# Kernel tuning notes

Hardware: AMD Instinct MI355X
Metric: run time of the kernel (lower is better)

The kernel has to match this reference:

```python
import jax, jax.numpy as jnp
import numpy as np

LAMB = 5.0
B, N = 1024, 3125  # batch, anchors (5 anchors x 25x25 map)

def setup_inputs() -> dict:
    key = jax.random.key(0)
    k1, k2, k3, k4 = jax.random.split(key, 4)
    return {
        "c_pred": jax.random.normal(k1, (B, N, 2), dtype=jnp.float32),
        "r_pred": jax.random.normal(k2, (B, N, 4), dtype=jnp.float32),
        "r_target": jax.random.normal(k3, (B, N, 4), dtype=jnp.float32),
        # anchor labels in {-1: ignore, 0: negative, 1: positive}
        "label": jax.random.randint(k4, (B, N), -1, 2, dtype=jnp.int32),
    }

def reference(c_pred, r_pred, r_target, label):
    dt = c_pred.dtype
    pos = (label == 1)
    neg = (label == 0)
    pos_cnt = pos.sum(axis=-1).astype(dt)  # [B]
    neg_cnt = neg.sum(axis=-1).astype(dt)

    # --- classification: masked 2-class cross-entropy, pos/neg balanced per batch ---
    logp = jax.nn.log_softmax(c_pred, axis=-1)  # [B, N, 2]
    ce_pos = -logp[..., 1]                      # CE when target class = 1
    ce_neg = -logp[..., 0]                      # CE when target class = 0
    pos_mean = jnp.where(pos_cnt > 0,
                         (ce_pos * pos).sum(axis=-1) / jnp.maximum(pos_cnt, 1.0), 0.0)
    neg_mean = (ce_neg * neg).sum(axis=-1) / jnp.maximum(neg_cnt, 1.0)
    c_loss = ((pos_mean + neg_mean) * 0.5).mean()

    d = r_pred - r_target
    a = jnp.abs(d)
    sl = jnp.where(a < 1.0, 0.5 * d * d, a - 0.5)  # [B, N, 4]
    # per-batch mean over pos_num*4 elements == masked mean of per-anchor coord-mean
    r_per = (sl.mean(axis=-1) * pos).sum(axis=-1) / jnp.maximum(pos_cnt, 1.0)
    r_loss = jnp.where(pos_cnt > 0, r_per, 0.0).mean()

    t_loss = c_loss + LAMB * r_loss
    return (c_loss, r_loss, t_loss)
```

## Files before the change

### kernel.cpp

```cpp
#include <hip/hip_runtime.h>

#define BATCH 1024
#define NANCH 3125
#define LAMB  5.0f
#define NBLK  (BATCH * 4)

__device__ __forceinline__ float wave_red_f(float v) {
    #pragma unroll
    for (int o = 32; o > 0; o >>= 1) v += __shfl_down(v, o, 64);
    return v;
}

__device__ __forceinline__ float lse2(float cx, float cy) {
    const float m = fmaxf(cx, cy);
    return m + __logf(1.f + __expf(-fabsf(cx - cy)));
}

__device__ __forceinline__ float sl1(float4 p, float4 t) {
    float s4 = 0.f, d, a;
    d = p.x - t.x; a = fabsf(d); s4 += (a < 1.f) ? 0.5f * d * d : a - 0.5f;
    d = p.y - t.y; a = fabsf(d); s4 += (a < 1.f) ? 0.5f * d * d : a - 0.5f;
    d = p.z - t.z; a = fabsf(d); s4 += (a < 1.f) ? 0.5f * d * d : a - 0.5f;
    d = p.w - t.w; a = fabsf(d); s4 += (a < 1.f) ? 0.5f * d * d : a - 0.5f;
    return s4 * 0.25f;
}

__global__ __launch_bounds__(256) void partial_kernel(
    const float* __restrict__ c_pred,
    const float* __restrict__ r_pred,
    const float* __restrict__ r_target,
    const int*   __restrict__ label,
    float*       __restrict__ partial)
{
    const int blk = blockIdx.x;
    const int b   = blk >> 2;
    const int s   = blk & 3;
    const int tid = threadIdx.x;
    const int u   = (s << 8) | tid;

    const int align0  = (4 - (b & 3)) & 3;
    const int ngroups = (NANCH - align0) >> 2;
    const int ntail   = NANCH - align0 - (ngroups << 2);

    const float*  crow = c_pred + (size_t)b * (NANCH * 2);
    const float4* rp   = (const float4*)(r_pred   + (size_t)b * NANCH * 4);
    const float4* rt   = (const float4*)(r_target + (size_t)b * NANCH * 4);
    const int*    lb   = label + (size_t)b * NANCH;

    float cp = 0.f, cn = 0.f, sl = 0.f, pc = 0.f, nc = 0.f;

    if (u < ngroups) {
        const int a = align0 + (u << 2);

        const int4   L   = *(const int4*)(lb + a);
        const float4 C01 = *(const float4*)(crow + 2 * a);
        const float4 C23 = *(const float4*)(crow + 2 * a + 4);

        const bool p0 = (L.x == 1), p1 = (L.y == 1), p2 = (L.z == 1), p3 = (L.w == 1);
        float4 P0, T0, P1, T1, P2, T2, P3, T3;
        if (p0) { P0 = rp[a];     T0 = rt[a];     }
        if (p1) { P1 = rp[a + 1]; T1 = rt[a + 1]; }
        if (p2) { P2 = rp[a + 2]; T2 = rt[a + 2]; }
        if (p3) { P3 = rp[a + 3]; T3 = rt[a + 3]; }

        const float e0 = lse2(C01.x, C01.y), e1 = lse2(C01.z, C01.w);
        const float e2 = lse2(C23.x, C23.y), e3 = lse2(C23.z, C23.w);
        const bool n0 = (L.x == 0), n1 = (L.y == 0), n2 = (L.z == 0), n3 = (L.w == 0);

        pc = (p0 ? 1.f : 0.f) + (p1 ? 1.f : 0.f) + (p2 ? 1.f : 0.f) + (p3 ? 1.f : 0.f);
        nc = (n0 ? 1.f : 0.f) + (n1 ? 1.f : 0.f) + (n2 ? 1.f : 0.f) + (n3 ? 1.f : 0.f);
        cp = (p0 ? (e0 - C01.y) : 0.f) + (p1 ? (e1 - C01.w) : 0.f)
           + (p2 ? (e2 - C23.y) : 0.f) + (p3 ? (e3 - C23.w) : 0.f);
        cn = (n0 ? (e0 - C01.x) : 0.f) + (n1 ? (e1 - C01.z) : 0.f)
           + (n2 ? (e2 - C23.x) : 0.f) + (n3 ? (e3 - C23.z) : 0.f);

        if (p0) sl += sl1(P0, T0);
        if (p1) sl += sl1(P1, T1);
        if (p2) sl += sl1(P2, T2);
        if (p3) sl += sl1(P3, T3);
    } else {
        const int k = u - ngroups;
        const int nextra = align0 + ntail;
        if (k < nextra) {
            const int a = (k < align0) ? k
                        : (align0 + (ngroups << 2) + (k - align0));
            const int   l  = lb[a];
            const float cx = crow[2 * a], cy = crow[2 * a + 1];
            const float e  = lse2(cx, cy);
            if (l == 1) {
                pc = 1.f; cp = e - cy;
                sl = sl1(rp[a], rt[a]);
            } else if (l == 0) {
                nc = 1.f; cn = e - cx;
            }
        }
    }

    cp = wave_red_f(cp);
    cn = wave_red_f(cn);
    sl = wave_red_f(sl);
    pc = wave_red_f(pc);
    nc = wave_red_f(nc);

    __shared__ float sm[5][4];
    const int wid = tid >> 6, lane = tid & 63;
    if (lane == 0) {
        sm[0][wid] = cp; sm[1][wid] = cn; sm[2][wid] = sl;
        sm[3][wid] = pc; sm[4][wid] = nc;
    }
    __syncthreads();
    if (tid < 5) {
        const int k = tid;
        partial[(size_t)blk * 5 + k] = sm[k][0] + sm[k][1] + sm[k][2] + sm[k][3];
    }
}

__global__ __launch_bounds__(512) void finalize_kernel(
    const float* __restrict__ partial,
    float*       __restrict__ out)
{
    const int tid = threadIdx.x;
    float csum = 0.f, rsum = 0.f;

    for (int b = tid; b < BATCH; b += 512) {
        float cp = 0.f, cn = 0.f, sl = 0.f, pc = 0.f, nc = 0.f;
        #pragma unroll
        for (int s = 0; s < 4; ++s) {
            const float* p = partial + ((size_t)b * 4 + s) * 5;
            cp += p[0]; cn += p[1]; sl += p[2]; pc += p[3]; nc += p[4];
        }
        const bool haspos = (pc > 0.5f);
        const float pos_mean = haspos ? cp / pc : 0.f;
        const float neg_mean = cn / fmaxf(nc, 1.f);
        csum += (pos_mean + neg_mean) * 0.5f;
        rsum += haspos ? sl / pc : 0.f;
    }

    csum = wave_red_f(csum);
    rsum = wave_red_f(rsum);

    __shared__ float s_c[8], s_r[8];
    const int wid = tid >> 6, lane = tid & 63;
    if (lane == 0) { s_c[wid] = csum; s_r[wid] = rsum; }
    __syncthreads();
    if (tid == 0) {
        float cs = 0.f, rs = 0.f;
        #pragma unroll
        for (int w = 0; w < 8; ++w) { cs += s_c[w]; rs += s_r[w]; }
        const float c_loss = cs / (float)BATCH;
        const float r_loss = rs / (float)BATCH;
        out[0] = c_loss;
        out[1] = r_loss;
        out[2] = c_loss + LAMB * r_loss;
    }
}

extern "C" void kernel_launch(void* const* d_in, const int* in_sizes, int n_in,
                              void* d_out, int out_size, void* d_ws, size_t ws_size,
                              hipStream_t stream) {
    const float* c_pred   = (const float*)d_in[0];
    const float* r_pred   = (const float*)d_in[1];
    const float* r_target = (const float*)d_in[2];
    const int*   label    = (const int*)d_in[3];
    float*       out      = (float*)d_out;
    float*       partial  = (float*)d_ws;

    partial_kernel<<<NBLK, 256, 0, stream>>>(c_pred, r_pred, r_target, label, partial);
    finalize_kernel<<<1, 512, 0, stream>>>(partial, out);
}
```

Measured before the change: 28.25 us.

## Use one 1024-thread block per batch and finish per-batch means in-kernel

Replaces the four 256-thread blocks per batch row with a single 1024-thread block per row. The per-batch loss terms (pos/neg means and the regression mean) are now computed inside the partial kernel, which writes one float2 per batch. The finalize kernel then only sums 1024 float2 values instead of reading 20 partials per batch. The goal is to cut partial-buffer traffic and finalize work, at the cost of larger blocks and a wave-level barrier used inside a divergent branch.

Measured after the change: 28.62 us. About the same (+1.3%).

```diff
diff --git a/kernel.cpp b/kernel.cpp
--- a/kernel.cpp
+++ b/kernel.cpp
@@ -3,7 +3,6 @@
 #define BATCH 1024
 #define NANCH 3125
 #define LAMB  5.0f
-#define NBLK  (BATCH * 4)
 
 __device__ __forceinline__ float wave_red_f(float v) {
     #pragma unroll
@@ -25,18 +24,15 @@
     return s4 * 0.25f;
 }
 
-__global__ __launch_bounds__(256) void partial_kernel(
+__global__ __launch_bounds__(1024) void partial_kernel(
     const float* __restrict__ c_pred,
     const float* __restrict__ r_pred,
     const float* __restrict__ r_target,
     const int*   __restrict__ label,
-    float*       __restrict__ partial)
+    float2*      __restrict__ per_batch)
 {
-    const int blk = blockIdx.x;
-    const int b   = blk >> 2;
-    const int s   = blk & 3;
+    const int b   = blockIdx.x;
     const int tid = threadIdx.x;
-    const int u   = (s << 8) | tid;
 
     const int align0  = (4 - (b & 3)) & 3;
     const int ngroups = (NANCH - align0) >> 2;
@@ -49,8 +45,8 @@
 
     float cp = 0.f, cn = 0.f, sl = 0.f, pc = 0.f, nc = 0.f;
 
-    if (u < ngroups) {
-        const int a = align0 + (u << 2);
+    if (tid < ngroups) {
+        const int a = align0 + (tid << 2);
 
         const int4   L   = *(const int4*)(lb + a);
         const float4 C01 = *(const float4*)(crow + 2 * a);
@@ -79,7 +75,7 @@
         if (p2) sl += sl1(P2, T2);
         if (p3) sl += sl1(P3, T3);
     } else {
-        const int k = u - ngroups;
+        const int k = tid - ngroups;
         const int nextra = align0 + ntail;
         if (k < nextra) {
             const int a = (k < align0) ? k
@@ -102,46 +98,60 @@
     pc = wave_red_f(pc);
     nc = wave_red_f(nc);
 
-    __shared__ float sm[5][4];
+    __shared__ float sm[5][16];
     const int wid = tid >> 6, lane = tid & 63;
     if (lane == 0) {
         sm[0][wid] = cp; sm[1][wid] = cn; sm[2][wid] = sl;
         sm[3][wid] = pc; sm[4][wid] = nc;
     }
     __syncthreads();
-    if (tid < 5) {
-        const int k = tid;
-        partial[(size_t)blk * 5 + k] = sm[k][0] + sm[k][1] + sm[k][2] + sm[k][3];
+
+    if (tid < 64) {
+        float v = (tid < 80) ? ((float*)sm)[tid] : 0.f;
+        v += __shfl_down(v, 8, 64);
+        v += __shfl_down(v, 4, 64);
+        v += __shfl_down(v, 2, 64);
+        v += __shfl_down(v, 1, 64);
+        __shared__ float tot[5];
+        if ((tid & 15) == 0 && tid < 64) tot[tid >> 4] = v;
+        if (tid < 16) {
+            float w = ((float*)sm)[64 + tid];
+            w += __shfl_down(w, 8, 64);
+            w += __shfl_down(w, 4, 64);
+            w += __shfl_down(w, 2, 64);
+            w += __shfl_down(w, 1, 64);
+            if (tid == 0) tot[4] = w;
+        }
+        __builtin_amdgcn_s_barrier();
+        if (tid == 0) {
+            const float tcp = tot[0], tcn = tot[1], tsl = tot[2];
+            const float tpc = tot[3], tnc = tot[4];
+            const bool  haspos   = (tpc > 0.5f);
+            const float pos_mean = haspos ? tcp / tpc : 0.f;
+            const float neg_mean = tcn / fmaxf(tnc, 1.f);
+            const float c_contrib = (pos_mean + neg_mean) * 0.5f;
+            const float r_contrib = haspos ? tsl / tpc : 0.f;
+            per_batch[b] = make_float2(c_contrib, r_contrib);
+        }
     }
 }
 
 __global__ __launch_bounds__(512) void finalize_kernel(
-    const float* __restrict__ partial,
-    float*       __restrict__ out)
+    const float2* __restrict__ per_batch,
+    float*        __restrict__ out)
 {
     const int tid = threadIdx.x;
-    float csum = 0.f, rsum = 0.f;
+    const float2 v0 = per_batch[tid];
+    const float2 v1 = per_batch[tid + 512];
+    float c = v0.x + v1.x;
+    float r = v0.y + v1.y;
 
-    for (int b = tid; b < BATCH; b += 512) {
-        float cp = 0.f, cn = 0.f, sl = 0.f, pc = 0.f, nc = 0.f;
-        #pragma unroll
-        for (int s = 0; s < 4; ++s) {
-            const float* p = partial + ((size_t)b * 4 + s) * 5;
-            cp += p[0]; cn += p[1]; sl += p[2]; pc += p[3]; nc += p[4];
-        }
-        const bool haspos = (pc > 0.5f);
-        const float pos_mean = haspos ? cp / pc : 0.f;
-        const float neg_mean = cn / fmaxf(nc, 1.f);
-        csum += (pos_mean + neg_mean) * 0.5f;
-        rsum += haspos ? sl / pc : 0.f;
-    }
-
-    csum = wave_red_f(csum);
-    rsum = wave_red_f(rsum);
+    c = wave_red_f(c);
+    r = wave_red_f(r);
 
     __shared__ float s_c[8], s_r[8];
     const int wid = tid >> 6, lane = tid & 63;
-    if (lane == 0) { s_c[wid] = csum; s_r[wid] = rsum; }
+    if (lane == 0) { s_c[wid] = c; s_r[wid] = r; }
     __syncthreads();
     if (tid == 0) {
         float cs = 0.f, rs = 0.f;
@@ -163,8 +173,8 @@
     const float* r_target = (const float*)d_in[2];
     const int*   label    = (const int*)d_in[3];
     float*       out      = (float*)d_out;
-    float*       partial  = (float*)d_ws;
+    float2*      per_batch = (float2*)d_ws;
 
-    partial_kernel<<<NBLK, 256, 0, stream>>>(c_pred, r_pred, r_target, label, partial);
-    finalize_kernel<<<1, 512, 0, stream>>>(partial, out);
+    partial_kernel<<<BATCH, 1024, 0, stream>>>(c_pred, r_pred, r_target, label, per_batch);
+    finalize_kernel<<<1, 512, 0, stream>>>(per_batch, out);
 }
```
